# Optimization experiments

Measured on AMD Instinct MI355X. Metric: run time of the kernel, lower is better.

Reference implementation:

```python
import jax, jax.numpy as jnp
import numpy as np

N = 100000      # nodes
E = 1600000     # edges (avg degree 16)
IN = 512        # in_channels
H = 256         # hidden_channels
L = 8           # num_layers
ALPHA = 0.1
THETA = 0.5


def setup_inputs() -> dict:
    key = jax.random.key(0)
    k0, k1, k2, k3 = jax.random.split(key, 4)
    x = jax.random.normal(k0, (N, IN), jnp.float32)
    edge_index = jax.random.randint(k1, (2, E), 0, N, dtype=jnp.int64)
    W_embed = jax.random.normal(k2, (IN, H), jnp.float32) / np.sqrt(IN)
    b_embed = jnp.zeros((H,), jnp.float32)
    W_convs = jax.random.normal(k3, (L, H, H), jnp.float32) / np.sqrt(H)
    return {"x": x, "edge_index": edge_index, "W_embed": W_embed,
            "b_embed": b_embed, "W_convs": W_convs}


def _gcn_norm(edge_index, n):
    # gcn_norm: A_hat = A + I, D^{-1/2} A_hat D^{-1/2}
    loop = jnp.arange(n, dtype=edge_index.dtype)
    row = jnp.concatenate([edge_index[0], loop])  # source
    col = jnp.concatenate([edge_index[1], loop])  # target
    ones = jnp.ones(row.shape[0], jnp.float32)
    deg = jax.ops.segment_sum(ones, col, num_segments=n)
    dinv = jnp.where(deg > 0, jax.lax.rsqrt(deg), 0.0)
    norm = dinv[row] * dinv[col]  # [E+N]
    return row, col, norm


def _propagate(x, row, col, norm, n):
    # SpMM: out[i] = sum_{(j->i)} norm_e * x[j]
    msgs = x[row] * norm[:, None]  # [E+N, H]
    return jax.ops.segment_sum(msgs, col, num_segments=n)


def _gcn2_conv(x, x0, row, col, norm, W, layer):
    beta = np.log(THETA / layer + 1.0)
    h = _propagate(x, row, col, norm, x.shape[0])
    h = (1.0 - ALPHA) * h + ALPHA * x0          # initial residual (shared_weights)
    return (1.0 - beta) * h + beta * (h @ W)    # identity mapping


def reference(x, edge_index, W_embed, b_embed, W_convs):
    n = x.shape[0]
    row, col, norm = _gcn_norm(edge_index, n)
    h = jax.nn.relu(x @ W_embed + b_embed)
    h0 = h
    for l in range(L - 1):
        h = _gcn2_conv(h, h0, row, col, norm, W_convs[l], layer=l + 1)
        h = jax.nn.relu(h)  # dropout is identity in eval mode
    h = _gcn2_conv(h, h0, row, col, norm, W_convs[L - 1], layer=L)
    return h
```

## Files before the change

kernel.cpp:

```cpp
#include <hip/hip_runtime.h>
#include <cmath>

#define NNODES 100000
#define NEDGES 1600000
#define INC 512
#define HC 256
#define NLAYERS 8

typedef _Float16 half8 __attribute__((ext_vector_type(8)));
typedef _Float16 half4v __attribute__((ext_vector_type(4)));
typedef float floatx4 __attribute__((ext_vector_type(4)));

typedef __attribute__((address_space(3))) unsigned int u32_lds;
typedef __attribute__((address_space(1))) unsigned int u32_glb;

struct __attribute__((aligned(8))) EdgeP { int s; float w; };

__device__ __forceinline__ EdgeP ldnt_edge(const EdgeP* p) {
  unsigned long long v = __builtin_nontemporal_load((const unsigned long long*)p);
  EdgeP e; __builtin_memcpy(&e, &v, 8); return e;
}
__device__ __forceinline__ half4v ldnt_h4(const _Float16* p) {
  unsigned long long v = __builtin_nontemporal_load((const unsigned long long*)p);
  half4v h; __builtin_memcpy(&h, &v, 8); return h;
}

__global__ void k_detect(const unsigned int* __restrict__ eb, int* __restrict__ mode) {
  int lane = threadIdx.x;
  unsigned v = eb[2 * lane + 1];
  unsigned long long nz = __ballot(v != 0u);
  if (lane == 0) *mode = (nz == 0ull) ? 1 : 0;
}

__device__ __forceinline__ int edge_at(const void* eb, int m, int i) {
  return m ? (int)((const long long*)eb)[i] : ((const int*)eb)[i];
}


__global__ __launch_bounds__(256) void k_zero2(int* __restrict__ a, int* __restrict__ b, int n) {
  int i = blockIdx.x * 256 + threadIdx.x;
  if (i < n) { a[i] = 0; b[i] = 0; }
}

__global__ __launch_bounds__(256) void k_count(const void* __restrict__ eb, const int* __restrict__ mode,
                                               int* __restrict__ counts) {
  int e = blockIdx.x * 256 + threadIdx.x;
  if (e >= NEDGES) return;
  int m = *mode;
  atomicAdd(&counts[edge_at(eb, m, NEDGES + e)], 1);
}

__global__ __launch_bounds__(256) void k_dinv(const int* __restrict__ counts, float* __restrict__ dinv) {
  int i = blockIdx.x * 256 + threadIdx.x;
  if (i < NNODES) dinv[i] = 1.0f / sqrtf((float)counts[i] + 1.0f);
}

__global__ __launch_bounds__(256) void k_scan1(const int* __restrict__ counts, int* __restrict__ rowptr,
                                               int* __restrict__ partials) {
  __shared__ int sm[256];
  int i = blockIdx.x * 256 + threadIdx.x;
  int v = (i < NNODES) ? counts[i] : 0;
  sm[threadIdx.x] = v;
  __syncthreads();
  for (int off = 1; off < 256; off <<= 1) {
    int u = (threadIdx.x >= off) ? sm[threadIdx.x - off] : 0;
    __syncthreads();
    sm[threadIdx.x] += u;
    __syncthreads();
  }
  if (i < NNODES) rowptr[i] = sm[threadIdx.x] - v;
  if (threadIdx.x == 255) partials[blockIdx.x] = sm[255];
}

__global__ __launch_bounds__(512) void k_scan2(int* __restrict__ partials, int* __restrict__ rowptr, int nb) {
  __shared__ int sm[512];
  int t = threadIdx.x;
  int v = (t < nb) ? partials[t] : 0;
  sm[t] = v;
  __syncthreads();
  for (int off = 1; off < 512; off <<= 1) {
    int u = (t >= off) ? sm[t - off] : 0;
    __syncthreads();
    sm[t] += u;
    __syncthreads();
  }
  if (t < nb) partials[t] = sm[t] - v;
  if (t == 0) rowptr[NNODES] = NEDGES;
}

__global__ __launch_bounds__(256) void k_scan3(int* __restrict__ rowptr, const int* __restrict__ partials) {
  int i = blockIdx.x * 256 + threadIdx.x;
  if (i < NNODES) rowptr[i] += partials[blockIdx.x];
}

__global__ __launch_bounds__(256) void k_fill(const void* __restrict__ eb, const int* __restrict__ mode,
                                              const int* __restrict__ rowptr,
                                              int* __restrict__ cursor, const float* __restrict__ dinv,
                                              EdgeP* __restrict__ ep) {
  int e = blockIdx.x * 256 + threadIdx.x;
  if (e >= NEDGES) return;
  int m = *mode;
  int r = edge_at(eb, m, e), c = edge_at(eb, m, NEDGES + e);
  int p = rowptr[c] + atomicAdd(&cursor[c], 1);
  EdgeP pr; pr.s = r; pr.w = dinv[r] * dinv[c];
  ep[p] = pr;
}

__global__ __launch_bounds__(256) void k_tr_wemb(const float* __restrict__ W, _Float16* __restrict__ WT) {
  int idx = blockIdx.x * 256 + threadIdx.x;
  int k = idx & 511, c = idx >> 9;
  WT[idx] = (_Float16)W[k * 256 + c];
}
__global__ __launch_bounds__(256) void k_tr_wc(const float* __restrict__ W, _Float16* __restrict__ WT) {
  int idx = blockIdx.x * 256 + threadIdx.x;
  int k = idx & 255, n = (idx >> 8) & 255, l = idx >> 16;
  WT[idx] = (_Float16)W[(l * 256 + k) * 256 + n];
}


__global__ __launch_bounds__(256) void k_embed(const float* __restrict__ X,
                                               const _Float16* __restrict__ WT,
                                               const float* __restrict__ bias,
                                               _Float16* __restrict__ outh, _Float16* __restrict__ outh2) {
  __shared__ char smem[16896];
  int t = threadIdx.x;
  int wave = t >> 6, lane = t & 63;
  int r = lane & 15, g = lane >> 4;
  int row0 = blockIdx.x * 64;
  int c0 = wave * 64;

  floatx4 acc[4][4] = {};

  auto stage = [&](int buf, int ks) {
#pragma unroll
    for (int rd = 0; rd < 2; ++rd) {
      int L = rd * 256 + t;
      int row = L >> 3;
      int u = (L & 7) ^ (row & 7);
      int grow = row0 + row; if (grow >= NNODES) grow = NNODES - 1;
      const float* src = X + (size_t)grow * INC + ks + u * 4;
      char* dstbase = smem + buf * 8192 + (rd * 256 + wave * 64) * 16;
      __builtin_amdgcn_global_load_lds((const u32_glb*)src, (u32_lds*)dstbase, 16, 0, 0);
    }
  };

  auto compute = [&](int buf, int ks) {
    const char* bufp = smem + buf * 8192;
    half8 a[4], b[4];
#pragma unroll
    for (int rt = 0; rt < 4; ++rt) {
      int row = rt * 16 + r;
      int sw = row & 7;
      float4 f0 = *(const float4*)(bufp + row * 128 + ((2 * g) ^ sw) * 16);
      float4 f1 = *(const float4*)(bufp + row * 128 + ((2 * g + 1) ^ sw) * 16);
      a[rt] = half8{ (_Float16)f0.x, (_Float16)f0.y, (_Float16)f0.z, (_Float16)f0.w,
                     (_Float16)f1.x, (_Float16)f1.y, (_Float16)f1.z, (_Float16)f1.w };
    }
#pragma unroll
    for (int ct = 0; ct < 4; ++ct)
      b[ct] = *(const half8*)(WT + (size_t)(c0 + ct * 16 + r) * INC + ks + g * 8);
#pragma unroll
    for (int rt = 0; rt < 4; ++rt)
#pragma unroll
      for (int ct = 0; ct < 4; ++ct)
        acc[rt][ct] = __builtin_amdgcn_mfma_f32_16x16x32_f16(a[rt], b[ct], acc[rt][ct], 0, 0, 0);
  };

  stage(0, 0);
#pragma unroll 2
  for (int s = 0; s < 16; ++s) {
    if (s < 15) stage((s + 1) & 1, (s + 1) * 32);
    __syncthreads();
    compute(s & 1, s * 32);
    __syncthreads();
  }

  _Float16 (*Cl)[264] = (_Float16(*)[264])smem;
#pragma unroll
  for (int p = 0; p < 2; ++p) {
    __syncthreads();
#pragma unroll
    for (int rt2 = 0; rt2 < 2; ++rt2) {
      int rt = p * 2 + rt2;
#pragma unroll
      for (int q = 0; q < 4; ++q) {
        int lrow = rt2 * 16 + g * 4 + q;
#pragma unroll
        for (int ct = 0; ct < 4; ++ct) {
          int col = c0 + ct * 16 + r;
          float v = acc[rt][ct][q] + bias[col];
          v = fmaxf(v, 0.0f);
          Cl[lrow][col] = (_Float16)v;
        }
      }
    }
    __syncthreads();
    int lrow = t >> 3, cc = (t & 7) * 32;
    int grow = row0 + p * 32 + lrow;
    if (grow < NNODES) {
      size_t base = (size_t)grow * HC + cc;
#pragma unroll
      for (int i = 0; i < 4; ++i) {
        half8 v = *(const half8*)&Cl[lrow][cc + i * 8];
        *(half8*)(outh + base + i * 8) = v;
        *(half8*)(outh2 + base + i * 8) = v;
      }
    }
  }
}


template <bool LAST>
__global__ __launch_bounds__(256) void k_layer(const _Float16* __restrict__ h,
                                               const _Float16* __restrict__ h0,
                                               const int* __restrict__ rowptr,
                                               const EdgeP* __restrict__ ep,
                                               const float* __restrict__ dinv,
                                               const _Float16* __restrict__ WT,
                                               float ob, float beta,
                                               _Float16* __restrict__ hn, float* __restrict__ outf) {
  __shared__ _Float16 M[32][264];
  int t = threadIdx.x;
  int wave = t >> 6, lane = t & 63;
  int row0 = blockIdx.x * 32;
  int c = lane * 4;

  for (int i = 0; i < 8; ++i) {
    int lrow = wave * 8 + i;
    int node = row0 + lrow;
    if (node < NNODES) {
      size_t base = (size_t)node * HC + c;
      float di = dinv[node];
      float wsw = di * di;
      half4v hv = *(const half4v*)(h + base);
      float a0 = wsw * (float)hv[0], a1 = wsw * (float)hv[1];
      float a2 = wsw * (float)hv[2], a3 = wsw * (float)hv[3];
      int e = rowptr[node], en = rowptr[node + 1];
      for (; e + 7 < en; e += 8) {
        EdgeP p0 = ldnt_edge(ep + e),     p1 = ldnt_edge(ep + e + 1);
        EdgeP p2 = ldnt_edge(ep + e + 2), p3 = ldnt_edge(ep + e + 3);
        EdgeP p4 = ldnt_edge(ep + e + 4), p5 = ldnt_edge(ep + e + 5);
        EdgeP p6 = ldnt_edge(ep + e + 6), p7 = ldnt_edge(ep + e + 7);
        half4v x0 = *(const half4v*)(h + (size_t)p0.s * HC + c);
        half4v x1 = *(const half4v*)(h + (size_t)p1.s * HC + c);
        half4v x2 = *(const half4v*)(h + (size_t)p2.s * HC + c);
        half4v x3 = *(const half4v*)(h + (size_t)p3.s * HC + c);
        half4v x4 = *(const half4v*)(h + (size_t)p4.s * HC + c);
        half4v x5 = *(const half4v*)(h + (size_t)p5.s * HC + c);
        half4v x6 = *(const half4v*)(h + (size_t)p6.s * HC + c);
        half4v x7 = *(const half4v*)(h + (size_t)p7.s * HC + c);
        a0 += p0.w * (float)x0[0] + p1.w * (float)x1[0] + p2.w * (float)x2[0] + p3.w * (float)x3[0]
            + p4.w * (float)x4[0] + p5.w * (float)x5[0] + p6.w * (float)x6[0] + p7.w * (float)x7[0];
        a1 += p0.w * (float)x0[1] + p1.w * (float)x1[1] + p2.w * (float)x2[1] + p3.w * (float)x3[1]
            + p4.w * (float)x4[1] + p5.w * (float)x5[1] + p6.w * (float)x6[1] + p7.w * (float)x7[1];
        a2 += p0.w * (float)x0[2] + p1.w * (float)x1[2] + p2.w * (float)x2[2] + p3.w * (float)x3[2]
            + p4.w * (float)x4[2] + p5.w * (float)x5[2] + p6.w * (float)x6[2] + p7.w * (float)x7[2];
        a3 += p0.w * (float)x0[3] + p1.w * (float)x1[3] + p2.w * (float)x2[3] + p3.w * (float)x3[3]
            + p4.w * (float)x4[3] + p5.w * (float)x5[3] + p6.w * (float)x6[3] + p7.w * (float)x7[3];
      }
      for (; e + 3 < en; e += 4) {
        EdgeP p0 = ldnt_edge(ep + e),     p1 = ldnt_edge(ep + e + 1);
        EdgeP p2 = ldnt_edge(ep + e + 2), p3 = ldnt_edge(ep + e + 3);
        half4v x0 = *(const half4v*)(h + (size_t)p0.s * HC + c);
        half4v x1 = *(const half4v*)(h + (size_t)p1.s * HC + c);
        half4v x2 = *(const half4v*)(h + (size_t)p2.s * HC + c);
        half4v x3 = *(const half4v*)(h + (size_t)p3.s * HC + c);
        a0 += p0.w * (float)x0[0] + p1.w * (float)x1[0] + p2.w * (float)x2[0] + p3.w * (float)x3[0];
        a1 += p0.w * (float)x0[1] + p1.w * (float)x1[1] + p2.w * (float)x2[1] + p3.w * (float)x3[1];
        a2 += p0.w * (float)x0[2] + p1.w * (float)x1[2] + p2.w * (float)x2[2] + p3.w * (float)x3[2];
        a3 += p0.w * (float)x0[3] + p1.w * (float)x1[3] + p2.w * (float)x2[3] + p3.w * (float)x3[3];
      }
      for (; e < en; ++e) {
        EdgeP p0 = ldnt_edge(ep + e);
        half4v x0 = *(const half4v*)(h + (size_t)p0.s * HC + c);
        a0 += p0.w * (float)x0[0];
        a1 += p0.w * (float)x0[1];
        a2 += p0.w * (float)x0[2];
        a3 += p0.w * (float)x0[3];
      }
      half4v h0v = ldnt_h4(h0 + base);
      half4v mo = { (_Float16)(0.9f * a0 + 0.1f * (float)h0v[0]),
                    (_Float16)(0.9f * a1 + 0.1f * (float)h0v[1]),
                    (_Float16)(0.9f * a2 + 0.1f * (float)h0v[2]),
                    (_Float16)(0.9f * a3 + 0.1f * (float)h0v[3]) };
      *(half4v*)&M[lrow][c] = mo;
    } else {
      *(half4v*)&M[lrow][c] = half4v{ (_Float16)0, (_Float16)0, (_Float16)0, (_Float16)0 };
    }
  }
  __syncthreads();

  int r = lane & 15, g = lane >> 4;
  int c0 = wave * 64;
  floatx4 acc[2][4] = {};
#pragma unroll
  for (int ks = 0; ks < HC; ks += 32) {
    half8 a[2], b[4];
    a[0] = *(const half8*)&M[r][ks + g * 8];
    a[1] = *(const half8*)&M[16 + r][ks + g * 8];
#pragma unroll
    for (int ct = 0; ct < 4; ++ct)
      b[ct] = *(const half8*)(WT + (size_t)(c0 + ct * 16 + r) * HC + ks + g * 8);
#pragma unroll
    for (int rt = 0; rt < 2; ++rt)
#pragma unroll
      for (int ct = 0; ct < 4; ++ct)
        acc[rt][ct] = __builtin_amdgcn_mfma_f32_16x16x32_f16(a[rt], b[ct], acc[rt][ct], 0, 0, 0);
  }
  __syncthreads();

#pragma unroll
  for (int rt = 0; rt < 2; ++rt) {
#pragma unroll
    for (int q = 0; q < 4; ++q) {
      int lrow = rt * 16 + g * 4 + q;
#pragma unroll
      for (int ct = 0; ct < 4; ++ct) {
        int col = c0 + ct * 16 + r;
        float v = ob * (float)M[lrow][col] + beta * acc[rt][ct][q];
        if constexpr (!LAST) {
          v = fmaxf(v, 0.0f);
          M[lrow][col] = (_Float16)v;
        } else {
          int row = row0 + lrow;
          if (row < NNODES) outf[(size_t)row * HC + col] = v;
        }
      }
    }
  }
  if constexpr (!LAST) {
    __syncthreads();
    int lrow = t >> 3, cc = (t & 7) * 32;
    int grow = row0 + lrow;
    if (grow < NNODES) {
      size_t base = (size_t)grow * HC + cc;
#pragma unroll
      for (int i = 0; i < 4; ++i)
        *(half8*)(hn + base + i * 8) = *(const half8*)&M[lrow][cc + i * 8];
    }
  }
}


extern "C" void kernel_launch(void* const* d_in, const int* in_sizes, int n_in,
                              void* d_out, int out_size, void* d_ws, size_t ws_size,
                              hipStream_t stream) {
  const float* x = (const float*)d_in[0];
  const void* ei = d_in[1];
  const float* wemb = (const float*)d_in[2];
  const float* bemb = (const float*)d_in[3];
  const float* wc = (const float*)d_in[4];
  (void)in_sizes; (void)n_in; (void)out_size; (void)ws_size;

  char* ws = (char*)d_ws;
  size_t o = 0;
  auto alloc = [&](size_t bytes) -> char* {
    char* p = ws + o;
    o = (o + bytes + 511) & ~(size_t)511;
    return p;
  };
  _Float16* hh      = (_Float16*)alloc((size_t)NNODES * HC * 2);
  _Float16* h0h     = (_Float16*)alloc((size_t)NNODES * HC * 2);
  EdgeP*    ep      = (EdgeP*)alloc((size_t)NEDGES * 8);
  _Float16* wembT   = (_Float16*)alloc((size_t)INC * HC * 2);
  _Float16* wcT     = (_Float16*)alloc((size_t)NLAYERS * HC * HC * 2);
  int*      counts  = (int*)alloc((size_t)NNODES * 4);
  int*      cursor  = (int*)alloc((size_t)NNODES * 4);
  int*      rowptr  = (int*)alloc((size_t)(NNODES + 1) * 4);
  float*    dinv    = (float*)alloc((size_t)NNODES * 4);
  int*      partials= (int*)alloc(2048);
  int*      mode    = (int*)alloc(256);
  _Float16* hd      = (_Float16*)d_out;

  const int NB = (NNODES + 255) / 256;
  const int GEMM_GRID = (NNODES + 63) / 64;
  const int LAYER_GRID = (NNODES + 31) / 32;

  k_detect<<<1, 64, 0, stream>>>((const unsigned int*)ei, mode);
  k_zero2<<<NB, 256, 0, stream>>>(counts, cursor, NNODES);
  k_tr_wemb<<<(INC * HC) / 256, 256, 0, stream>>>(wemb, wembT);
  k_tr_wc<<<(NLAYERS * HC * HC) / 256, 256, 0, stream>>>(wc, wcT);
  k_count<<<(NEDGES + 255) / 256, 256, 0, stream>>>(ei, mode, counts);
  k_dinv<<<NB, 256, 0, stream>>>(counts, dinv);
  k_scan1<<<NB, 256, 0, stream>>>(counts, rowptr, partials);
  k_scan2<<<1, 512, 0, stream>>>(partials, rowptr, NB);
  k_scan3<<<NB, 256, 0, stream>>>(rowptr, partials);
  k_fill<<<(NEDGES + 255) / 256, 256, 0, stream>>>(ei, mode, rowptr, cursor, dinv, ep);

  k_embed<<<GEMM_GRID, 256, 0, stream>>>(x, wembT, bemb, hd, h0h);

  _Float16* cur = hd;
  _Float16* nxt = hh;
  for (int l = 0; l < NLAYERS; ++l) {
    float beta = (float)log(0.5 / (double)(l + 1) + 1.0);
    float ob = 1.0f - beta;
    const _Float16* W = wcT + (size_t)l * HC * HC;
    if (l < NLAYERS - 1) {
      k_layer<false><<<LAYER_GRID, 256, 0, stream>>>(cur, h0h, rowptr, ep, dinv, W,
                                                     ob, beta, nxt, (float*)nullptr);
      _Float16* tmp = cur; cur = nxt; nxt = tmp;
    } else {
      k_layer<true><<<LAYER_GRID, 256, 0, stream>>>(cur, h0h, rowptr, ep, dinv, W,
                                                    ob, beta, (_Float16*)nullptr, (float*)d_out);
    }
  }
}
```

Baseline: 1.954 ms.

## Gather with 16-byte loads, two nodes per wave, predicated 8-edge batches

The SpMM gather in the fused layer kernel is remapped so each wave handles two nodes at once, with 32 lanes per node each loading 8 halves (16 bytes) instead of 4. The 8/4/1 edge-loop cascade becomes a single 8-wide batch loop whose tail edges are predicated with zero weights, which lets more gather loads be in flight. Nontemporal loads for edges and h0 are replaced with ordinary loads. The risks are wasted loads on padded tail edges, lane divergence between the two nodes sharing a wave, and higher register pressure from the 8 accumulators.

```diff
diff --git a/kernel.cpp b/kernel.cpp
--- a/kernel.cpp
+++ b/kernel.cpp
@@ -15,15 +15,6 @@
 typedef __attribute__((address_space(1))) unsigned int u32_glb;
 
 struct __attribute__((aligned(8))) EdgeP { int s; float w; };
-
-__device__ __forceinline__ EdgeP ldnt_edge(const EdgeP* p) {
-  unsigned long long v = __builtin_nontemporal_load((const unsigned long long*)p);
-  EdgeP e; __builtin_memcpy(&e, &v, 8); return e;
-}
-__device__ __forceinline__ half4v ldnt_h4(const _Float16* p) {
-  unsigned long long v = __builtin_nontemporal_load((const unsigned long long*)p);
-  half4v h; __builtin_memcpy(&h, &v, 8); return h;
-}
 
 __global__ void k_detect(const unsigned int* __restrict__ eb, int* __restrict__ mode) {
   int lane = threadIdx.x;
@@ -222,77 +213,53 @@
   __shared__ _Float16 M[32][264];
   int t = threadIdx.x;
   int wave = t >> 6, lane = t & 63;
+  int half = lane >> 5;
+  int lc = lane & 31;
+  int c8 = lc * 8;
   int row0 = blockIdx.x * 32;
-  int c = lane * 4;
-
-  for (int i = 0; i < 8; ++i) {
-    int lrow = wave * 8 + i;
+
+  for (int p = 0; p < 4; ++p) {
+    int lrow = wave * 8 + p * 2 + half;
     int node = row0 + lrow;
-    if (node < NNODES) {
-      size_t base = (size_t)node * HC + c;
-      float di = dinv[node];
-      float wsw = di * di;
-      half4v hv = *(const half4v*)(h + base);
-      float a0 = wsw * (float)hv[0], a1 = wsw * (float)hv[1];
-      float a2 = wsw * (float)hv[2], a3 = wsw * (float)hv[3];
-      int e = rowptr[node], en = rowptr[node + 1];
-      for (; e + 7 < en; e += 8) {
-        EdgeP p0 = ldnt_edge(ep + e),     p1 = ldnt_edge(ep + e + 1);
-        EdgeP p2 = ldnt_edge(ep + e + 2), p3 = ldnt_edge(ep + e + 3);
-        EdgeP p4 = ldnt_edge(ep + e + 4), p5 = ldnt_edge(ep + e + 5);
-        EdgeP p6 = ldnt_edge(ep + e + 6), p7 = ldnt_edge(ep + e + 7);
-        half4v x0 = *(const half4v*)(h + (size_t)p0.s * HC + c);
-        half4v x1 = *(const half4v*)(h + (size_t)p1.s * HC + c);
-        half4v x2 = *(const half4v*)(h + (size_t)p2.s * HC + c);
-        half4v x3 = *(const half4v*)(h + (size_t)p3.s * HC + c);
-        half4v x4 = *(const half4v*)(h + (size_t)p4.s * HC + c);
-        half4v x5 = *(const half4v*)(h + (size_t)p5.s * HC + c);
-        half4v x6 = *(const half4v*)(h + (size_t)p6.s * HC + c);
-        half4v x7 = *(const half4v*)(h + (size_t)p7.s * HC + c);
-        a0 += p0.w * (float)x0[0] + p1.w * (float)x1[0] + p2.w * (float)x2[0] + p3.w * (float)x3[0]
-            + p4.w * (float)x4[0] + p5.w * (float)x5[0] + p6.w * (float)x6[0] + p7.w * (float)x7[0];
-        a1 += p0.w * (float)x0[1] + p1.w * (float)x1[1] + p2.w * (float)x2[1] + p3.w * (float)x3[1]
-            + p4.w * (float)x4[1] + p5.w * (float)x5[1] + p6.w * (float)x6[1] + p7.w * (float)x7[1];
-        a2 += p0.w * (float)x0[2] + p1.w * (float)x1[2] + p2.w * (float)x2[2] + p3.w * (float)x3[2]
-            + p4.w * (float)x4[2] + p5.w * (float)x5[2] + p6.w * (float)x6[2] + p7.w * (float)x7[2];
-        a3 += p0.w * (float)x0[3] + p1.w * (float)x1[3] + p2.w * (float)x2[3] + p3.w * (float)x3[3]
-            + p4.w * (float)x4[3] + p5.w * (float)x5[3] + p6.w * (float)x6[3] + p7.w * (float)x7[3];
+    bool valid = node < NNODES;
+    int cn = valid ? node : NNODES - 1;
+    size_t base = (size_t)cn * HC + c8;
+    float di = dinv[cn];
+    float wsw = valid ? di * di : 0.0f;
+    half8 hv = *(const half8*)(h + base);
+    float acc[8];
+#pragma unroll
+    for (int j = 0; j < 8; ++j) acc[j] = wsw * (float)hv[j];
+    int e = rowptr[cn];
+    int en = valid ? rowptr[cn + 1] : e;
+    for (; e < en; e += 8) {
+#pragma unroll
+      for (int k2 = 0; k2 < 8; ++k2) {
+        int idx = e + k2;
+        bool v2 = idx < en;
+        EdgeP pk = ep[v2 ? idx : en - 1];
+        float w = v2 ? pk.w : 0.0f;
+        half8 x = *(const half8*)(h + (size_t)pk.s * HC + c8);
+#pragma unroll
+        for (int j = 0; j < 8; ++j) acc[j] += w * (float)x[j];
       }
-      for (; e + 3 < en; e += 4) {
-        EdgeP p0 = ldnt_edge(ep + e),     p1 = ldnt_edge(ep + e + 1);
-        EdgeP p2 = ldnt_edge(ep + e + 2), p3 = ldnt_edge(ep + e + 3);
-        half4v x0 = *(const half4v*)(h + (size_t)p0.s * HC + c);
-        half4v x1 = *(const half4v*)(h + (size_t)p1.s * HC + c);
-        half4v x2 = *(const half4v*)(h + (size_t)p2.s * HC + c);
-        half4v x3 = *(const half4v*)(h + (size_t)p3.s * HC + c);
-        a0 += p0.w * (float)x0[0] + p1.w * (float)x1[0] + p2.w * (float)x2[0] + p3.w * (float)x3[0];
-        a1 += p0.w * (float)x0[1] + p1.w * (float)x1[1] + p2.w * (float)x2[1] + p3.w * (float)x3[1];
-        a2 += p0.w * (float)x0[2] + p1.w * (float)x1[2] + p2.w * (float)x2[2] + p3.w * (float)x3[2];
-        a3 += p0.w * (float)x0[3] + p1.w * (float)x1[3] + p2.w * (float)x2[3] + p3.w * (float)x3[3];
-      }
-      for (; e < en; ++e) {
-        EdgeP p0 = ldnt_edge(ep + e);
-        half4v x0 = *(const half4v*)(h + (size_t)p0.s * HC + c);
-        a0 += p0.w * (float)x0[0];
-        a1 += p0.w * (float)x0[1];
-        a2 += p0.w * (float)x0[2];
-        a3 += p0.w * (float)x0[3];
-      }
-      half4v h0v = ldnt_h4(h0 + base);
-      half4v mo = { (_Float16)(0.9f * a0 + 0.1f * (float)h0v[0]),
-                    (_Float16)(0.9f * a1 + 0.1f * (float)h0v[1]),
-                    (_Float16)(0.9f * a2 + 0.1f * (float)h0v[2]),
-                    (_Float16)(0.9f * a3 + 0.1f * (float)h0v[3]) };
-      *(half4v*)&M[lrow][c] = mo;
+    }
+    half8 h0v = *(const half8*)(h0 + base);
+    half8 mo;
+#pragma unroll
+    for (int j = 0; j < 8; ++j) mo[j] = (_Float16)(0.9f * acc[j] + 0.1f * (float)h0v[j]);
+    if (valid) {
+      *(half8*)&M[lrow][c8] = mo;
     } else {
-      *(half4v*)&M[lrow][c] = half4v{ (_Float16)0, (_Float16)0, (_Float16)0, (_Float16)0 };
+      half8 z = {};
+      *(half8*)&M[lrow][c8] = z;
     }
   }
   __syncthreads();
 
   int r = lane & 15, g = lane >> 4;
   int c0 = wave * 64;
-  floatx4 acc[2][4] = {};
+  floatx4 acc2[2][4] = {};
 #pragma unroll
   for (int ks = 0; ks < HC; ks += 32) {
     half8 a[2], b[4];
@@ -305,7 +272,7 @@
     for (int rt = 0; rt < 2; ++rt)
 #pragma unroll
       for (int ct = 0; ct < 4; ++ct)
-        acc[rt][ct] = __builtin_amdgcn_mfma_f32_16x16x32_f16(a[rt], b[ct], acc[rt][ct], 0, 0, 0);
+        acc2[rt][ct] = __builtin_amdgcn_mfma_f32_16x16x32_f16(a[rt], b[ct], acc2[rt][ct], 0, 0, 0);
   }
   __syncthreads();
 
@@ -317,7 +284,7 @@
 #pragma unroll
       for (int ct = 0; ct < 4; ++ct) {
         int col = c0 + ct * 16 + r;
-        float v = ob * (float)M[lrow][col] + beta * acc[rt][ct][q];
+        float v = ob * (float)M[lrow][col] + beta * acc2[rt][ct][q];
         if constexpr (!LAST) {
           v = fmaxf(v, 0.0f);
           M[lrow][col] = (_Float16)v;
```

Result: faster. 1.703 ms, median of 2 (-12.8%).
